# Performance work log

Hardware: AMD Instinct MI355X
Metric: run time of the kernel (lower is better)

The kernel has to match this reference:

```python
import jax, jax.numpy as jnp
import numpy as np

N_NODES = 100000
N_EDGES = 3200000
OUT_FEATURES = 128


def setup_inputs() -> dict:
    key = jax.random.key(0)
    k1, k2, k3, k4, k5 = jax.random.split(key, 5)
    edge_row = jax.random.randint(k1, (N_EDGES,), 0, N_NODES, dtype=jnp.int32)
    edge_col = jax.random.randint(k2, (N_EDGES,), 0, N_NODES, dtype=jnp.int32)
    edge_val = jax.random.uniform(k3, (N_EDGES,), dtype=jnp.float32)
    stdv = 1.0 / np.sqrt(OUT_FEATURES)
    weight = jax.random.uniform(k4, (N_NODES, OUT_FEATURES), minval=-stdv, maxval=stdv, dtype=jnp.float32)
    bias = jax.random.uniform(k5, (OUT_FEATURES,), minval=-stdv, maxval=stdv, dtype=jnp.float32)
    return {"edge_row": edge_row, "edge_col": edge_col, "edge_val": edge_val,
            "weight": weight, "bias": bias}


def reference(edge_row, edge_col, edge_val, weight, bias):
    # SpMM: out = adj @ weight, adj given in COO (row, col, val), shape [N, N]
    n_nodes = weight.shape[0]
    gathered = edge_val[:, None] * weight[edge_col]            # [E, F]
    out = jax.ops.segment_sum(gathered, edge_row, num_segments=n_nodes)  # [N, F]
    return out + bias
```

## Files before the change

kernel.cpp:

```cpp
#include <hip/hip_runtime.h>

#define F 128
#define RB 64
#define RB_SHIFT 6
#define CAP 4096
#define SCH 4096
#define PT3 1024
#define EPT3 (SCH / PT3)
#define NSEG 8
#define COL_BITS 17
#define COL_MASK 0x1FFFF
#define MAXNB 2048

__global__ __launch_bounds__(256) void cvt_chist_kernel(
    const float4* __restrict__ w4, uint* __restrict__ wq32, float* __restrict__ scales,
    int total4, const int* __restrict__ rows, int* __restrict__ cntmat, int n_edges,
    int nb, int nchunks) {
    if ((int)blockIdx.x < nchunks) {
        __shared__ int h[MAXNB];
        int c = blockIdx.x, t = threadIdx.x;
        for (int i = t; i < nb; i += 256) h[i] = 0;
        __syncthreads();
        int e0 = c * SCH, e1 = min(e0 + SCH, n_edges);
        if (e1 - e0 == SCH) {
            const int4* r4 = (const int4*)(rows + e0);
#pragma unroll
            for (int k = 0; k < 4; k++) {
                int4 rv = r4[k * 256 + t];
                atomicAdd(&h[rv.x >> RB_SHIFT], 1);
                atomicAdd(&h[rv.y >> RB_SHIFT], 1);
                atomicAdd(&h[rv.z >> RB_SHIFT], 1);
                atomicAdd(&h[rv.w >> RB_SHIFT], 1);
            }
        } else {
            for (int e = e0 + t; e < e1; e += 256) atomicAdd(&h[rows[e] >> RB_SHIFT], 1);
        }
        __syncthreads();
        for (int i = t; i < nb; i += 256) cntmat[(size_t)c * nb + i] = h[i];
    } else {
        int idx = (blockIdx.x - nchunks) * 256 + threadIdx.x;
        if (idx >= total4) return;
        float4 f = w4[idx];
        float m = fmaxf(fmaxf(fabsf(f.x), fabsf(f.y)), fmaxf(fabsf(f.z), fabsf(f.w)));
#pragma unroll
        for (int off = 1; off <= 16; off <<= 1) m = fmaxf(m, __shfl_xor(m, off));
        float inv = m > 0.f ? 127.f / m : 0.f;
        int q0 = (int)rintf(f.x * inv) + 128;
        int q1 = (int)rintf(f.y * inv) + 128;
        int q2 = (int)rintf(f.z * inv) + 128;
        int q3 = (int)rintf(f.w * inv) + 128;
        wq32[idx] = (uint)(q0 | (q1 << 8) | (q2 << 16) | (q3 << 24));
        if ((idx & 31) == 0) scales[idx >> 5] = m * (1.f / 127.f);
    }
}

__global__ __launch_bounds__(256) void scanA_kernel(int* __restrict__ cntmat,
                                                    int* __restrict__ segsum,
                                                    int nb, int nchunks) {
    int b = blockIdx.x * 256 + threadIdx.x;
    if (b >= nb) return;
    int sg = blockIdx.y;
    int cps = (nchunks + NSEG - 1) / NSEG;
    int c0 = sg * cps, c1 = min(c0 + cps, nchunks);
    int run = 0;
#pragma unroll 4
    for (int c = c0; c < c1; c++) {
        int v = cntmat[(size_t)c * nb + b];
        cntmat[(size_t)c * nb + b] = run;
        run += v;
    }
    segsum[sg * nb + b] = run;
}

__global__ void scanBC_kernel(int* __restrict__ segsum, int* __restrict__ boffs, int nb) {
    __shared__ int lds[1024];
    int t = threadIdx.x;
    int per = (nb + 1023) / 1024;
    int base = t * per;
    int cnt[2] = {0, 0};
    int s = 0;
    for (int i = 0; i < per && i < 2; i++) {
        int b = base + i;
        int run = 0;
        if (b < nb) {
            for (int sg = 0; sg < NSEG; sg++) {
                int v = segsum[sg * nb + b];
                segsum[sg * nb + b] = run;
                run += v;
            }
        }
        cnt[i] = run;
        s += run;
    }
    lds[t] = s;
    __syncthreads();
    for (int off = 1; off < 1024; off <<= 1) {
        int a = (t >= off) ? lds[t - off] : 0;
        __syncthreads();
        lds[t] += a;
        __syncthreads();
    }
    int excl = lds[t] - s;
    for (int i = 0; i < per && i < 2; i++) {
        int b = base + i;
        if (b < nb) {
            boffs[b] = excl;
            excl += cnt[i];
        }
    }
    if (t == 1023) boffs[nb] = lds[1023];
}

__global__ __launch_bounds__(PT3) void scatter_kernel(
    const int* __restrict__ rows, const int* __restrict__ cols,
    const float* __restrict__ vals, const float* __restrict__ scales,
    const int* __restrict__ boffs, const int* __restrict__ segsum,
    const int* __restrict__ cntmat, int2* __restrict__ epk, int n_edges, int nb,
    int nchunks) {
    __shared__ int relc[MAXNB];
    __shared__ int hist[MAXNB];
    __shared__ int lcur[MAXNB];
    __shared__ int2 buf[SCH];
    __shared__ ushort sbkt[SCH];
    __shared__ int wsum[PT3 / 64], wbase[PT3 / 64];
    int t = threadIdx.x;
    int lane = t & 63, w = t >> 6;
    int cps = (nchunks + NSEG - 1) / NSEG;
    int c = blockIdx.x;

    int e0 = c * SCH, e1 = min(e0 + SCH, n_edges);
    int cnt = e1 - e0;
    int sg = c / cps;

    for (int i = t; i < nb; i += PT3) {
        relc[i] = boffs[i] + segsum[sg * nb + i] + cntmat[(size_t)c * nb + i];
        hist[i] = 0;
    }
    __syncthreads();

    int er[EPT3], ec[EPT3];
    float ev[EPT3];
    int eb = e0 + (t << 2);
    if (eb + 4 <= e1) {
        int4 rv = *(const int4*)(rows + eb);
        int4 cv = *(const int4*)(cols + eb);
        float4 vv = *(const float4*)(vals + eb);
        er[0] = rv.x; er[1] = rv.y; er[2] = rv.z; er[3] = rv.w;
        ec[0] = cv.x; ec[1] = cv.y; ec[2] = cv.z; ec[3] = cv.w;
        ev[0] = vv.x * scales[ec[0]];
        ev[1] = vv.y * scales[ec[1]];
        ev[2] = vv.z * scales[ec[2]];
        ev[3] = vv.w * scales[ec[3]];
#pragma unroll
        for (int k = 0; k < 4; k++) atomicAdd(&hist[er[k] >> RB_SHIFT], 1);
    } else {
#pragma unroll
        for (int k = 0; k < 4; k++) {
            int e = eb + k;
            if (e < e1) {
                er[k] = rows[e];
                ec[k] = cols[e];
                ev[k] = vals[e] * scales[ec[k]];
                atomicAdd(&hist[er[k] >> RB_SHIFT], 1);
            }
        }
    }
    __syncthreads();

    int b0 = t << 1;
    int h0 = (b0 + 0 < nb) ? hist[b0 + 0] : 0;
    int h1 = (b0 + 1 < nb) ? hist[b0 + 1] : 0;
    int psum = h0 + h1;
    int v = psum;
#pragma unroll
    for (int off = 1; off < 64; off <<= 1) {
        int a = __shfl_up(v, off);
        if (lane >= off) v += a;
    }
    if (lane == 63) wsum[w] = v;
    __syncthreads();
    if (t == 0) {
        int run = 0;
        for (int i = 0; i < PT3 / 64; i++) {
            wbase[i] = run;
            run += wsum[i];
        }
    }
    __syncthreads();
    int excl = v - psum + wbase[w];
    if (b0 + 0 < nb) { lcur[b0 + 0] = excl; relc[b0 + 0] -= excl; }
    excl += h0;
    if (b0 + 1 < nb) { lcur[b0 + 1] = excl; relc[b0 + 1] -= excl; }
    __syncthreads();

#pragma unroll
    for (int k = 0; k < EPT3; k++) {
        int e = eb + k;
        if (e < e1) {
            int b = er[k] >> RB_SHIFT;
            int p = atomicAdd(&lcur[b], 1);
            buf[p] = make_int2(ec[k] | ((er[k] & (RB - 1)) << COL_BITS),
                               __float_as_int(ev[k]));
            sbkt[p] = (ushort)b;
        }
    }
    __syncthreads();

    for (int i = t; i < cnt; i += PT3) epk[relc[sbkt[i]] + i] = buf[i];
}

__global__ __launch_bounds__(512, 8) void sortacc_kernel(
    const int* __restrict__ boffs, const int2* __restrict__ epk,
    const uint* __restrict__ wq32, const float* __restrict__ bias,
    float* __restrict__ out, int n_nodes) {
    __shared__ int2 buf[CAP];
    __shared__ int hist[RB], lstart[RB], lcur[RB];
    int b = blockIdx.x;
    int s = boffs[b];
    int cnt = boffs[b + 1] - s;
    int row0 = b << RB_SHIFT;
    int t = threadIdx.x;
    int lane = t & 63, w = t >> 6;
    int half = lane >> 5;
    int c32 = lane & 31;
    float4 bb4 = ((const float4*)bias)[c32];

#define B0(u) ((float)((u) & 0xFFu))
#define B1(u) ((float)(((u) >> 8) & 0xFFu))
#define B2(u) ((float)(((u) >> 16) & 0xFFu))
#define B3(u) ((float)((u) >> 24))

    if (cnt <= CAP) {
        if (t < RB) hist[t] = 0;
        __syncthreads();
        int2 r0, r1, r2, r3, r4, r5, r6, r7;
#define LOADK(rk, k)                                                     \
        {                                                                \
            int i = t + (k)*512;                                         \
            if (i < cnt) {                                               \
                rk = epk[s + i];                                         \
                atomicAdd(&hist[(unsigned)rk.x >> COL_BITS], 1);         \
            }                                                            \
        }
        LOADK(r0, 0) LOADK(r1, 1) LOADK(r2, 2) LOADK(r3, 3)
        LOADK(r4, 4) LOADK(r5, 5) LOADK(r6, 6) LOADK(r7, 7)
#undef LOADK
        __syncthreads();
        if (w == 0) {
            int hv = hist[lane];
            int v = hv;
#pragma unroll
            for (int off = 1; off < 64; off <<= 1) {
                int a = __shfl_up(v, off);
                if (lane >= off) v += a;
            }
            lstart[lane] = v - hv;
            lcur[lane] = v - hv;
        }
        __syncthreads();
#define SCATK(rk, k)                                                         \
        {                                                                    \
            int i = t + (k)*512;                                             \
            if (i < cnt) {                                                   \
                int p = atomicAdd(&lcur[(unsigned)rk.x >> COL_BITS], 1);     \
                buf[p] = make_int2((int)(((uint)rk.x & COL_MASK) << 5), rk.y);\
            }                                                                \
        }
        SCATK(r0, 0) SCATK(r1, 1) SCATK(r2, 2) SCATK(r3, 3)
        SCATK(r4, 4) SCATK(r5, 5) SCATK(r6, 6) SCATK(r7, 7)
#undef SCATK
        __syncthreads();

        for (int j = 0; j < 8; j++) {
            int rl = w * 8 + j;
            int gr = row0 + rl;
            if (gr >= n_nodes) break;
            int e = lstart[rl];
            int end = e + hist[rl];
            float ax0 = 0.f, ax1 = 0.f, ax2 = 0.f, ax3 = 0.f, sv = 0.f;
            for (; e + 12 <= end; e += 12) {
                int2 p0 = buf[e + 0 + half], p1 = buf[e + 2 + half];
                int2 p2 = buf[e + 4 + half], p3 = buf[e + 6 + half];
                int2 p4 = buf[e + 8 + half], p5 = buf[e + 10 + half];
                uint u0 = wq32[(uint)p0.x + c32];
                uint u1 = wq32[(uint)p1.x + c32];
                uint u2 = wq32[(uint)p2.x + c32];
                uint u3 = wq32[(uint)p3.x + c32];
                uint u4 = wq32[(uint)p4.x + c32];
                uint u5 = wq32[(uint)p5.x + c32];
                float v0 = __int_as_float(p0.y), v1 = __int_as_float(p1.y);
                float v2 = __int_as_float(p2.y), v3 = __int_as_float(p3.y);
                float v4 = __int_as_float(p4.y), v5 = __int_as_float(p5.y);
                ax0 += v0 * B0(u0) + v1 * B0(u1) + v2 * B0(u2) + v3 * B0(u3) +
                       v4 * B0(u4) + v5 * B0(u5);
                ax1 += v0 * B1(u0) + v1 * B1(u1) + v2 * B1(u2) + v3 * B1(u3) +
                       v4 * B1(u4) + v5 * B1(u5);
                ax2 += v0 * B2(u0) + v1 * B2(u1) + v2 * B2(u2) + v3 * B2(u3) +
                       v4 * B2(u4) + v5 * B2(u5);
                ax3 += v0 * B3(u0) + v1 * B3(u1) + v2 * B3(u2) + v3 * B3(u3) +
                       v4 * B3(u4) + v5 * B3(u5);
                sv += ((v0 + v1) + (v2 + v3)) + (v4 + v5);
            }
            for (; e + 2 <= end; e += 2) {
                int2 pk = buf[e + half];
                uint u = wq32[(uint)pk.x + c32];
                float v = __int_as_float(pk.y);
                ax0 += v * B0(u);
                ax1 += v * B1(u);
                ax2 += v * B2(u);
                ax3 += v * B3(u);
                sv += v;
            }
            if (e < end && half == 0) {
                int2 pk = buf[e];
                uint u = wq32[(uint)pk.x + c32];
                float v = __int_as_float(pk.y);
                ax0 += v * B0(u);
                ax1 += v * B1(u);
                ax2 += v * B2(u);
                ax3 += v * B3(u);
                sv += v;
            }
            ax0 += __shfl_xor(ax0, 32);
            ax1 += __shfl_xor(ax1, 32);
            ax2 += __shfl_xor(ax2, 32);
            ax3 += __shfl_xor(ax3, 32);
            sv += __shfl_xor(sv, 32);
            if (half == 0) {
                float corr = 128.f * sv;
                ((float4*)out)[(size_t)gr * 32 + c32] =
                    make_float4(ax0 - corr + bb4.x, ax1 - corr + bb4.y,
                                ax2 - corr + bb4.z, ax3 - corr + bb4.w);
            }
        }
    } else {
        for (int j = 0; j < 8; j++) {
            int rl = w * 8 + j;
            int gr = row0 + rl;
            if (gr >= n_nodes) break;
            float ax0 = 0.f, ax1 = 0.f, ax2 = 0.f, ax3 = 0.f, sv = 0.f;
            if (half == 0) {
                for (int e = s; e < s + cnt; ++e) {
                    int2 pk = epk[e];
                    if ((int)((unsigned)pk.x >> COL_BITS) == rl) {
                        uint u = wq32[(((uint)pk.x & COL_MASK) << 5) + c32];
                        float v = __int_as_float(pk.y);
                        ax0 += v * B0(u);
                        ax1 += v * B1(u);
                        ax2 += v * B2(u);
                        ax3 += v * B3(u);
                        sv += v;
                    }
                }
            }
            ax0 += __shfl_xor(ax0, 32);
            ax1 += __shfl_xor(ax1, 32);
            ax2 += __shfl_xor(ax2, 32);
            ax3 += __shfl_xor(ax3, 32);
            sv += __shfl_xor(sv, 32);
            if (half == 0) {
                float corr = 128.f * sv;
                ((float4*)out)[(size_t)gr * 32 + c32] =
                    make_float4(ax0 - corr + bb4.x, ax1 - corr + bb4.y,
                                ax2 - corr + bb4.z, ax3 - corr + bb4.w);
            }
        }
    }
#undef B0
#undef B1
#undef B2
#undef B3
}

__global__ void init_out_kernel(float* __restrict__ out, const float* __restrict__ bias,
                                int n_nodes) {
    const float4* b4 = (const float4*)bias;
    float4* o4 = (float4*)out;
    int total = n_nodes * (F / 4);
    for (int i = blockIdx.x * blockDim.x + threadIdx.x; i < total;
         i += gridDim.x * blockDim.x)
        o4[i] = b4[i & (F / 4 - 1)];
}

__global__ void edge_scatter_kernel(const int* __restrict__ rows,
                                    const int* __restrict__ cols,
                                    const float* __restrict__ vals,
                                    const float* __restrict__ weight,
                                    float* __restrict__ out, int n_edges) {
    int e = (blockIdx.x * blockDim.x + threadIdx.x) >> 6;
    if (e >= n_edges) return;
    int lane = threadIdx.x & 63;
    float2 w = ((const float2*)(weight + (size_t)cols[e] * F))[lane];
    float val = vals[e];
    float* o = out + (size_t)rows[e] * F + lane * 2;
    unsafeAtomicAdd(o, val * w.x);
    unsafeAtomicAdd(o + 1, val * w.y);
}

extern "C" void kernel_launch(void* const* d_in, const int* in_sizes, int n_in,
                              void* d_out, int out_size, void* d_ws, size_t ws_size,
                              hipStream_t stream) {
    const int*   rows   = (const int*)d_in[0];
    const int*   cols   = (const int*)d_in[1];
    const float* vals   = (const float*)d_in[2];
    const float* weight = (const float*)d_in[3];
    const float* bias   = (const float*)d_in[4];
    float* out = (float*)d_out;

    int n_edges = in_sizes[0];
    int n_nodes = out_size / F;
    int nb = (n_nodes + RB - 1) / RB;
    int nchunks = (n_edges + SCH - 1) / SCH;

    size_t head_ints  = ((size_t)nb + 2) & ~(size_t)1;
    size_t epk_off    = head_ints * 4;
    size_t scales_off = epk_off + (size_t)n_edges * 8;
    size_t wq_off     = (scales_off + (size_t)n_nodes * 4 + 255) & ~(size_t)255;
    size_t mat_off    = (wq_off + (size_t)n_nodes * F + 255) & ~(size_t)255;
    size_t seg_off    = mat_off + (size_t)nchunks * nb * 4;
    size_t need       = seg_off + (size_t)NSEG * nb * 4;

    if (ws_size < need || n_nodes > (1 << COL_BITS) || nb > MAXNB) {
        init_out_kernel<<<2048, 256, 0, stream>>>(out, bias, n_nodes);
        int grid = (n_edges + 3) / 4;
        edge_scatter_kernel<<<grid, 256, 0, stream>>>(rows, cols, vals, weight, out,
                                                      n_edges);
        return;
    }

    int* boffs    = (int*)d_ws;
    int2* epk     = (int2*)((char*)d_ws + epk_off);
    float* scales = (float*)((char*)d_ws + scales_off);
    uint* wq32    = (uint*)((char*)d_ws + wq_off);
    int* cntmat   = (int*)((char*)d_ws + mat_off);
    int* segsum   = (int*)((char*)d_ws + seg_off);

    int total4 = n_nodes * (F / 4);
    int cvt_blocks = (total4 + 255) / 256;
    cvt_chist_kernel<<<nchunks + cvt_blocks, 256, 0, stream>>>(
        (const float4*)weight, wq32, scales, total4, rows, cntmat, n_edges, nb, nchunks);
    dim3 ga((nb + 255) / 256, NSEG);
    scanA_kernel<<<ga, 256, 0, stream>>>(cntmat, segsum, nb, nchunks);
    scanBC_kernel<<<1, 1024, 0, stream>>>(segsum, boffs, nb);
    scatter_kernel<<<nchunks, PT3, 0, stream>>>(rows, cols, vals, scales, boffs, segsum,
                                                cntmat, epk, n_edges, nb, nchunks);
    sortacc_kernel<<<nb, 512, 0, stream>>>(boffs, epk, wq32, bias, out, n_nodes);
}
```

Measured before the change: 145.6 us.

## Sort edges by column quarter within row block to improve weight gather locality

The in-block counting sort now keys each edge on (column quarter, local row), with four column ranges, so each block walks column quarter by quarter. Within a quarter, all 64 rows of the block gather from one quarter of the quantized weight table, so concurrently running blocks hit a narrower address range and should get better L2/MALL reuse. Each warp keeps per-row accumulators for its 8 rows in registers across the quarters and writes them out at the end. The cost is more registers (40 accumulators per thread against a 512x8 launch bound), a shorter unroll of 6 instead of 12 edges, and four times as many short segments, each with its own tail handling.

```diff
diff --git a/kernel.cpp b/kernel.cpp
--- a/kernel.cpp
+++ b/kernel.cpp
@@ -11,6 +11,9 @@
 #define COL_BITS 17
 #define COL_MASK 0x1FFFF
 #define MAXNB 2048
+#define NQ 4
+#define QSHIFT 15
+#define NKEY (NQ * RB)
 
 __global__ __launch_bounds__(256) void cvt_chist_kernel(
     const float4* __restrict__ w4, uint* __restrict__ wq32, float* __restrict__ scales,
@@ -214,7 +217,7 @@
     const uint* __restrict__ wq32, const float* __restrict__ bias,
     float* __restrict__ out, int n_nodes) {
     __shared__ int2 buf[CAP];
-    __shared__ int hist[RB], lstart[RB], lcur[RB];
+    __shared__ int hist[NKEY], lstart[NKEY], lcur[NKEY];
     int b = blockIdx.x;
     int s = boffs[b];
     int cnt = boffs[b + 1] - s;
@@ -229,9 +232,10 @@
 #define B1(u) ((float)(((u) >> 8) & 0xFFu))
 #define B2(u) ((float)(((u) >> 16) & 0xFFu))
 #define B3(u) ((float)((u) >> 24))
+#define KEY(px) (((((uint)(px) >> QSHIFT) & (NQ - 1)) << RB_SHIFT) | ((uint)(px) >> COL_BITS))
 
     if (cnt <= CAP) {
-        if (t < RB) hist[t] = 0;
+        if (t < NKEY) hist[t] = 0;
         __syncthreads();
         int2 r0, r1, r2, r3, r4, r5, r6, r7;
 #define LOADK(rk, k)                                                     \
@@ -239,7 +243,7 @@
             int i = t + (k)*512;                                         \
             if (i < cnt) {                                               \
                 rk = epk[s + i];                                         \
-                atomicAdd(&hist[(unsigned)rk.x >> COL_BITS], 1);         \
+                atomicAdd(&hist[KEY(rk.x)], 1);                          \
             }                                                            \
         }
         LOADK(r0, 0) LOADK(r1, 1) LOADK(r2, 2) LOADK(r3, 3)
@@ -247,22 +251,27 @@
 #undef LOADK
         __syncthreads();
         if (w == 0) {
-            int hv = hist[lane];
-            int v = hv;
+            int k0 = lane << 2;
+            int h0 = hist[k0], h1 = hist[k0 + 1], h2 = hist[k0 + 2], h3 = hist[k0 + 3];
+            int psum = h0 + h1 + h2 + h3;
+            int v = psum;
 #pragma unroll
             for (int off = 1; off < 64; off <<= 1) {
                 int a = __shfl_up(v, off);
                 if (lane >= off) v += a;
             }
-            lstart[lane] = v - hv;
-            lcur[lane] = v - hv;
+            int excl = v - psum;
+            lstart[k0] = excl; lcur[k0] = excl; excl += h0;
+            lstart[k0 + 1] = excl; lcur[k0 + 1] = excl; excl += h1;
+            lstart[k0 + 2] = excl; lcur[k0 + 2] = excl; excl += h2;
+            lstart[k0 + 3] = excl; lcur[k0 + 3] = excl;
         }
         __syncthreads();
 #define SCATK(rk, k)                                                         \
         {                                                                    \
             int i = t + (k)*512;                                             \
             if (i < cnt) {                                                   \
-                int p = atomicAdd(&lcur[(unsigned)rk.x >> COL_BITS], 1);     \
+                int p = atomicAdd(&lcur[KEY(rk.x)], 1);                      \
                 buf[p] = make_int2((int)(((uint)rk.x & COL_MASK) << 5), rk.y);\
             }                                                                \
         }
@@ -271,66 +280,66 @@
 #undef SCATK
         __syncthreads();
 
+        float ax0[8], ax1[8], ax2[8], ax3[8], svs[8];
+#pragma unroll
         for (int j = 0; j < 8; j++) {
-            int rl = w * 8 + j;
-            int gr = row0 + rl;
-            if (gr >= n_nodes) break;
-            int e = lstart[rl];
-            int end = e + hist[rl];
-            float ax0 = 0.f, ax1 = 0.f, ax2 = 0.f, ax3 = 0.f, sv = 0.f;
-            for (; e + 12 <= end; e += 12) {
-                int2 p0 = buf[e + 0 + half], p1 = buf[e + 2 + half];
-                int2 p2 = buf[e + 4 + half], p3 = buf[e + 6 + half];
-                int2 p4 = buf[e + 8 + half], p5 = buf[e + 10 + half];
-                uint u0 = wq32[(uint)p0.x + c32];
-                uint u1 = wq32[(uint)p1.x + c32];
-                uint u2 = wq32[(uint)p2.x + c32];
-                uint u3 = wq32[(uint)p3.x + c32];
-                uint u4 = wq32[(uint)p4.x + c32];
-                uint u5 = wq32[(uint)p5.x + c32];
-                float v0 = __int_as_float(p0.y), v1 = __int_as_float(p1.y);
-                float v2 = __int_as_float(p2.y), v3 = __int_as_float(p3.y);
-                float v4 = __int_as_float(p4.y), v5 = __int_as_float(p5.y);
-                ax0 += v0 * B0(u0) + v1 * B0(u1) + v2 * B0(u2) + v3 * B0(u3) +
-                       v4 * B0(u4) + v5 * B0(u5);
-                ax1 += v0 * B1(u0) + v1 * B1(u1) + v2 * B1(u2) + v3 * B1(u3) +
-                       v4 * B1(u4) + v5 * B1(u5);
-                ax2 += v0 * B2(u0) + v1 * B2(u1) + v2 * B2(u2) + v3 * B2(u3) +
-                       v4 * B2(u4) + v5 * B2(u5);
-                ax3 += v0 * B3(u0) + v1 * B3(u1) + v2 * B3(u2) + v3 * B3(u3) +
-                       v4 * B3(u4) + v5 * B3(u5);
-                sv += ((v0 + v1) + (v2 + v3)) + (v4 + v5);
-            }
-            for (; e + 2 <= end; e += 2) {
-                int2 pk = buf[e + half];
-                uint u = wq32[(uint)pk.x + c32];
-                float v = __int_as_float(pk.y);
-                ax0 += v * B0(u);
-                ax1 += v * B1(u);
-                ax2 += v * B2(u);
-                ax3 += v * B3(u);
-                sv += v;
-            }
-            if (e < end && half == 0) {
-                int2 pk = buf[e];
-                uint u = wq32[(uint)pk.x + c32];
-                float v = __int_as_float(pk.y);
-                ax0 += v * B0(u);
-                ax1 += v * B1(u);
-                ax2 += v * B2(u);
-                ax3 += v * B3(u);
-                sv += v;
-            }
-            ax0 += __shfl_xor(ax0, 32);
-            ax1 += __shfl_xor(ax1, 32);
-            ax2 += __shfl_xor(ax2, 32);
-            ax3 += __shfl_xor(ax3, 32);
-            sv += __shfl_xor(sv, 32);
-            if (half == 0) {
+            ax0[j] = 0.f; ax1[j] = 0.f; ax2[j] = 0.f; ax3[j] = 0.f; svs[j] = 0.f;
+        }
+        for (int q = 0; q < NQ; q++) {
+#pragma unroll
+            for (int j = 0; j < 8; j++) {
+                int key = (q << RB_SHIFT) | (w * 8 + j);
+                int e = lstart[key];
+                int end = e + hist[key];
+                float a0 = 0.f, a1 = 0.f, a2 = 0.f, a3 = 0.f, sv = 0.f;
+                for (; e + 6 <= end; e += 6) {
+                    int2 p0 = buf[e + 0 + half];
+                    int2 p1 = buf[e + 2 + half];
+                    int2 p2 = buf[e + 4 + half];
+                    uint u0 = wq32[(uint)p0.x + c32];
+                    uint u1 = wq32[(uint)p1.x + c32];
+                    uint u2 = wq32[(uint)p2.x + c32];
+                    float v0 = __int_as_float(p0.y);
+                    float v1 = __int_as_float(p1.y);
+                    float v2 = __int_as_float(p2.y);
+                    a0 += v0 * B0(u0) + v1 * B0(u1) + v2 * B0(u2);
+                    a1 += v0 * B1(u0) + v1 * B1(u1) + v2 * B1(u2);
+                    a2 += v0 * B2(u0) + v1 * B2(u1) + v2 * B2(u2);
+                    a3 += v0 * B3(u0) + v1 * B3(u1) + v2 * B3(u2);
+                    sv += (v0 + v1) + v2;
+                }
+                for (; e + 2 <= end; e += 2) {
+                    int2 pk = buf[e + half];
+                    uint u = wq32[(uint)pk.x + c32];
+                    float v = __int_as_float(pk.y);
+                    a0 += v * B0(u); a1 += v * B1(u);
+                    a2 += v * B2(u); a3 += v * B3(u);
+                    sv += v;
+                }
+                if (e < end && half == 0) {
+                    int2 pk = buf[e];
+                    uint u = wq32[(uint)pk.x + c32];
+                    float v = __int_as_float(pk.y);
+                    a0 += v * B0(u); a1 += v * B1(u);
+                    a2 += v * B2(u); a3 += v * B3(u);
+                    sv += v;
+                }
+                ax0[j] += a0; ax1[j] += a1; ax2[j] += a2; ax3[j] += a3; svs[j] += sv;
+            }
+        }
+#pragma unroll
+        for (int j = 0; j < 8; j++) {
+            int gr = row0 + w * 8 + j;
+            float a0 = ax0[j] + __shfl_xor(ax0[j], 32);
+            float a1 = ax1[j] + __shfl_xor(ax1[j], 32);
+            float a2 = ax2[j] + __shfl_xor(ax2[j], 32);
+            float a3 = ax3[j] + __shfl_xor(ax3[j], 32);
+            float sv = svs[j] + __shfl_xor(svs[j], 32);
+            if (gr < n_nodes && half == 0) {
                 float corr = 128.f * sv;
                 ((float4*)out)[(size_t)gr * 32 + c32] =
-                    make_float4(ax0 - corr + bb4.x, ax1 - corr + bb4.y,
-                                ax2 - corr + bb4.z, ax3 - corr + bb4.w);
+                    make_float4(a0 - corr + bb4.x, a1 - corr + bb4.y,
+                                a2 - corr + bb4.z, a3 - corr + bb4.w);
             }
         }
     } else {
@@ -338,31 +347,29 @@
             int rl = w * 8 + j;
             int gr = row0 + rl;
             if (gr >= n_nodes) break;
-            float ax0 = 0.f, ax1 = 0.f, ax2 = 0.f, ax3 = 0.f, sv = 0.f;
+            float a0 = 0.f, a1 = 0.f, a2 = 0.f, a3 = 0.f, sv = 0.f;
             if (half == 0) {
                 for (int e = s; e < s + cnt; ++e) {
                     int2 pk = epk[e];
                     if ((int)((unsigned)pk.x >> COL_BITS) == rl) {
                         uint u = wq32[(((uint)pk.x & COL_MASK) << 5) + c32];
                         float v = __int_as_float(pk.y);
-                        ax0 += v * B0(u);
-                        ax1 += v * B1(u);
-                        ax2 += v * B2(u);
-                        ax3 += v * B3(u);
+                        a0 += v * B0(u); a1 += v * B1(u);
+                        a2 += v * B2(u); a3 += v * B3(u);
                         sv += v;
                     }
                 }
             }
-            ax0 += __shfl_xor(ax0, 32);
-            ax1 += __shfl_xor(ax1, 32);
-            ax2 += __shfl_xor(ax2, 32);
-            ax3 += __shfl_xor(ax3, 32);
+            a0 += __shfl_xor(a0, 32);
+            a1 += __shfl_xor(a1, 32);
+            a2 += __shfl_xor(a2, 32);
+            a3 += __shfl_xor(a3, 32);
             sv += __shfl_xor(sv, 32);
             if (half == 0) {
                 float corr = 128.f * sv;
                 ((float4*)out)[(size_t)gr * 32 + c32] =
-                    make_float4(ax0 - corr + bb4.x, ax1 - corr + bb4.y,
-                                ax2 - corr + bb4.z, ax3 - corr + bb4.w);
+                    make_float4(a0 - corr + bb4.x, a1 - corr + bb4.y,
+                                a2 - corr + bb4.z, a3 - corr + bb4.w);
             }
         }
     }
@@ -370,6 +377,7 @@
 #undef B1
 #undef B2
 #undef B3
+#undef KEY
 }
 
 __global__ void init_out_kernel(float* __restrict__ out, const float* __restrict__ bias,
```

After: 306.4 us. 110% more time.
